# Performance work log

Hardware: AMD Instinct MI355X
Metric: run time of the kernel (lower is better)

The kernel has to match this reference:

```python
import jax, jax.numpy as jnp
import numpy as np

B, C, H, W = 4, 256, 64, 64
NB = 4            # num_bands
CR = C // 4       # channel-attention reduction


def _conv(x, w, b, pad):
    y = jax.lax.conv_general_dilated(x, w, window_strides=(1, 1),
                                     padding=[(pad, pad), (pad, pad)],
                                     dimension_numbers=('NCHW', 'OIHW', 'NCHW'))
    return y + b[None, :, None, None]


def setup_inputs() -> dict:
    key = jax.random.key(0)
    ks = jax.random.split(key, 16)
    d = {}
    d['x'] = jax.random.normal(ks[0], (B, C, H, W), dtype=jnp.float32)
    # spline weights / scalers: one (out,in) matrix per band
    d['spline_w'] = jax.random.normal(ks[1], (NB, C, C), dtype=jnp.float32) / np.sqrt(C)
    d['scalers'] = jax.random.uniform(ks[2], (NB, C, C), minval=0.9, maxval=1.1, dtype=jnp.float32)
    # feature_transform: conv3x3 -> BN -> ReLU -> conv3x3
    d['ft_w1'] = jax.random.normal(ks[3], (C, C, 3, 3), dtype=jnp.float32) / np.sqrt(C * 9)
    d['ft_b1'] = jnp.zeros((C,), jnp.float32)
    d['bn_g'] = jnp.ones((C,), jnp.float32)
    d['bn_b'] = jnp.zeros((C,), jnp.float32)
    d['bn_m'] = 0.01 * jax.random.normal(ks[4], (C,), dtype=jnp.float32)
    d['bn_v'] = jnp.ones((C,), jnp.float32)
    d['ft_w2'] = jax.random.normal(ks[5], (C, C, 3, 3), dtype=jnp.float32) / np.sqrt(C * 9)
    d['ft_b2'] = jnp.zeros((C,), jnp.float32)
    # channel attention: 1x1 convs C -> C/4 -> C
    d['ca_w1'] = jax.random.normal(ks[6], (CR, C, 1, 1), dtype=jnp.float32) / np.sqrt(C)
    d['ca_b1'] = jnp.zeros((CR,), jnp.float32)
    d['ca_w2'] = jax.random.normal(ks[7], (C, CR, 1, 1), dtype=jnp.float32) / np.sqrt(CR)
    d['ca_b2'] = jnp.zeros((C,), jnp.float32)
    # spatial attention: conv3x3 2 -> 1
    d['sa_w'] = jax.random.normal(ks[8], (1, 2, 3, 3), dtype=jnp.float32) / np.sqrt(18)
    d['sa_b'] = jnp.zeros((1,), jnp.float32)
    return d


def _forward(x, spline_w, scalers, ft_w1, ft_b1, bn_g, bn_b, bn_m, bn_v,
             ft_w2, ft_b2, ca_w1, ca_b1, ca_w2, ca_b2, sa_w, sa_b):
    eps = 1e-5

    def feature_transform(t):
        t = _conv(t, ft_w1, ft_b1, 1)
        t = bn_g[None, :, None, None] * (t - bn_m[None, :, None, None]) * \
            jax.lax.rsqrt(bn_v + eps)[None, :, None, None] + bn_b[None, :, None, None]
        t = jax.nn.relu(t)
        return _conv(t, ft_w2, ft_b2, 1)

    # ---- spectral decompose: rfft over channel dim, per-band irfft ----
    xf = x.transpose(0, 2, 3, 1).reshape(-1, C)      # (B*H*W, C)
    F = jnp.fft.rfft(xf, axis=-1)                    # (B*H*W, C//2+1)
    nfreq = F.shape[-1]
    bs = nfreq // NB
    bands = []
    for i in range(NB):
        s = i * bs
        e = nfreq if i == NB - 1 else (i + 1) * bs
        # irfft zero-pads the sliced spectrum back to length C (matches torch)
        bands.append(jnp.fft.irfft(F[:, s:e], n=C, axis=-1).reshape(B, H, W, C))
    xd = jnp.stack(bands, axis=1)                    # (B, NB, H, W, C)

    # NOTE: the original .view(B*NB, C, H, W) on a (B,NB,H,W,C)-contiguous tensor
    # is a raw memory reinterpretation (not a permute); jnp.reshape matches it.
    xd = xd.reshape(B * NB, C, H, W)
    xd = feature_transform(xd)
    xd = xd.reshape(B, NB, H, W, C)

    # ---- attention block (shares feature_transform weights) ----
    t = xd.reshape(B * NB, C, H, W)
    t = feature_transform(t)
    gap = jnp.mean(t, axis=(2, 3), keepdims=True)    # (B*NB, C, 1, 1)
    cw = jax.nn.sigmoid(_conv(jax.nn.gelu(_conv(gap, ca_w1, ca_b1, 0), approximate=False),
                              ca_w2, ca_b2, 0))
    t = t * cw
    avg_out = jnp.mean(t, axis=1, keepdims=True)
    max_out = jnp.max(t, axis=1, keepdims=True)
    sw = jax.nn.sigmoid(_conv(jnp.concatenate([avg_out, max_out], axis=1), sa_w, sa_b, 1))
    t = t * sw
    xd = t.reshape(B, NB, H, W, C)

    # ---- spline stage ----
    # In the source, the Cox-de Boor basis recursion is computed but UNUSED:
    # einsum('bci,oi->bci', band_x, weight) == band_x * weight.sum(0), so the
    # effective math is a per-band, per-feature scaling (dead basis code omitted).
    w_eff = (spline_w * scalers).sum(axis=1)          # (NB, C)
    xv = xd.reshape(B, NB, H * W, C)
    band_out = xv * w_eff[None, :, None, :]
    fused = band_out.mean(axis=1)                     # (B, H*W, C)
    return fused.reshape(B, H, W, C).transpose(0, 3, 1, 2)


def reference(x, spline_w, scalers, ft_w1, ft_b1, bn_g, bn_b, bn_m, bn_v,
              ft_w2, ft_b2, ca_w1, ca_b1, ca_w2, ca_b2, sa_w, sa_b):
    return _forward(x, spline_w, scalers, ft_w1, ft_b1, bn_g, bn_b, bn_m, bn_v,
                    ft_w2, ft_b2, ca_w1, ca_b1, ca_w2, ca_b2, sa_w, sa_b)
```

## Files before the change

kernel.cpp:

```cpp
#include <hip/hip_runtime.h>
#include <hip/hip_bf16.h>


#define CHW   1048576
#define HW    4096

typedef _Float16 f16;
typedef _Float16 f16x8 __attribute__((ext_vector_type(8)));
typedef float    f32x4 __attribute__((ext_vector_type(4)));

__global__ __launch_bounds__(256) void k2_kernel(float* __restrict__ K2) {
    __shared__ float ctab[256];
    const int c = blockIdx.x;
    const int t = threadIdx.x;
    ctab[t] = cosf((float)t * 0.024543692606170259f);
    __syncthreads();
#pragma unroll
    for (int q = 0; q < 4; q++) {
        const int o = q * 256 + t;
        const int s = q * 32;
        const int L = (q == 3) ? 33 : 32;
        float sum = ctab[(s * c) & 255];
        for (int k = 1; k < L; k++) {
            int m = ((s + k) * c + k * (256 - t)) & 255;
            sum += 2.f * ctab[m];
        }
        K2[c * 1024 + o] = sum * 0.00390625f;
    }
}

__global__ __launch_bounds__(256) void wsplit_kernel(const float* __restrict__ w,
                                                     f16* __restrict__ Wf) {
    const int tap = blockIdx.x / 16;
    const int ocgrp = blockIdx.x % 16;
    const int l = threadIdx.x & 63;
    const int c2 = threadIdx.x >> 6;
    const int lrow = l & 15, icg = l >> 4;
    const int oc = ocgrp * 16 + lrow;
#pragma unroll
    for (int s = 0; s < 2; ++s) {
        const int cc = c2 + s * 4;
        const int icb = cc * 32 + icg * 8;
        f16x8 hi, lo;
#pragma unroll
        for (int j = 0; j < 8; ++j) {
            float v = w[(oc * 256 + icb + j) * 9 + tap];
            f16 h = (f16)v;
            hi[j] = h;
            lo[j] = (f16)(v - (float)h);
        }
        const size_t base = (((size_t)(tap * 8 + cc) * 2) * 16 + ocgrp) * 512 +
                            (size_t)l * 8;
        *(f16x8*)&Wf[base] = hi;
        *(f16x8*)&Wf[base + 8192] = lo;
    }
}

__global__ __launch_bounds__(256) void small_pre_kernel(
    const float* __restrict__ spw, const float* __restrict__ scl,
    const float* __restrict__ bn_g, const float* __restrict__ bn_b,
    const float* __restrict__ bn_m, const float* __restrict__ bn_v,
    const float* __restrict__ ft_b1, float* __restrict__ weff,
    float* __restrict__ bnscale, float* __restrict__ bnbias) {
    const int c = threadIdx.x;
    const float s = bn_g[c] * rsqrtf(bn_v[c] + 1e-5f);
    bnscale[c] = s;
    bnbias[c] = (ft_b1[c] - bn_m[c]) * s + bn_b[c];
    for (int n = 0; n < 4; n++) {
        float acc = 0.f;
        for (int j = 0; j < 256; j++)
            acc += spw[n * 65536 + j * 256 + c] * scl[n * 65536 + j * 256 + c];
        weff[n * 256 + c] = acc;
    }
}

__global__ __launch_bounds__(256) void decompose_kernel(const float* __restrict__ x,
                                                        const float* __restrict__ K2,
                                                        float* __restrict__ xd) {
    const int o0 = blockIdx.x * 128;
    const int p0 = blockIdx.y * 64;
    const int b = p0 >> 12;
    const int prow = p0 & 4095;
    const int t = threadIdx.x;
    const int pg = t >> 4, og = t & 15;
    __shared__ float As[16][64];
    __shared__ float Bs[16][128];
    float acc[4][8];
#pragma unroll
    for (int i = 0; i < 4; i++)
#pragma unroll
        for (int j = 0; j < 8; j++) acc[i][j] = 0.f;

    for (int c0 = 0; c0 < 256; c0 += 16) {
#pragma unroll
        for (int i = 0; i < 4; i++) {
            int c = (t >> 6) + i * 4;
            As[c][t & 63] = x[b * CHW + (c0 + c) * HW + prow + (t & 63)];
        }
#pragma unroll
        for (int i = 0; i < 8; i++) {
            int l = i * 256 + t;
            Bs[l >> 7][l & 127] = K2[(c0 + (l >> 7)) * 1024 + o0 + (l & 127)];
        }
        __syncthreads();
#pragma unroll
        for (int k = 0; k < 16; k++) {
            float a[4], bb[8];
            *(float4*)a = *(const float4*)&As[k][pg * 4];
            *(float4*)&bb[0] = *(const float4*)&Bs[k][og * 8];
            *(float4*)&bb[4] = *(const float4*)&Bs[k][og * 8 + 4];
#pragma unroll
            for (int i = 0; i < 4; i++)
#pragma unroll
                for (int j = 0; j < 8; j++) acc[i][j] = fmaf(a[i], bb[j], acc[i][j]);
        }
        __syncthreads();
    }
#pragma unroll
    for (int i = 0; i < 4; i++) {
        const int p = prow + pg * 4 + i;
#pragma unroll
        for (int j = 0; j < 8; j++) {
            const int o = o0 + og * 8 + j;
            const int n = o >> 8, cc = o & 255;
            xd[b * 4194304 + n * CHW + p * 256 + cc] = acc[i][j];
        }
    }
}

__global__ __launch_bounds__(256) void xpose_kernel(const float* __restrict__ in,
                                                    f16* __restrict__ Xh,
                                                    f16* __restrict__ Xl) {
    const int bn = blockIdx.y;
    const int tid = blockIdx.x;
    const int k = tid & 15;
    const int cc0 = ((tid >> 4) & 1) * 128;
    const int c0p = (tid >> 5) * 64;
    __shared__ float T[64 * 132];
    const int base = bn * 1048576;
    for (int c = threadIdx.x; c < 2048; c += 256) {
        int cl = c >> 5;
        int ccq = c & 31;
        int pd = (c0p + cl) * 16 + k;
        *(float4*)&T[cl * 132 + ccq * 4] =
            *(const float4*)&in[base + pd * 256 + cc0 + ccq * 4];
    }
    __syncthreads();
    for (int m = threadIdx.x; m < 1024; m += 256) {
        int pl = m >> 3;
        int cq = m & 7;
        f16x8 hi, lo;
#pragma unroll
        for (int j = 0; j < 8; ++j) {
            float v = T[(cq * 8 + j) * 132 + pl];
            f16 h = (f16)v;
            hi[j] = h;
            lo[j] = (f16)(v - (float)h);
        }
        int pp = k * 256 + cc0 + pl;
        int o = base + pp * 256 + c0p + cq * 8;
        *(f16x8*)&Xh[o] = hi;
        *(f16x8*)&Xl[o] = lo;
    }
}

template <int MODE, int PACKED>
__global__ __launch_bounds__(256, 2) void conv_mfma_kernel(
    const f16* __restrict__ Xh, const f16* __restrict__ Xl,
    const f16* __restrict__ Wf,
    const float* __restrict__ scale, const float* __restrict__ bias,
    f16* __restrict__ Oh, f16* __restrict__ Ol, float* __restrict__ Of) {
    const int oc0 = blockIdx.x * 128;
    const int h0 = (blockIdx.y >> 2) * 8;
    const int w0 = (blockIdx.y & 3) * 16;
    const int bn = blockIdx.z;

    __shared__ __align__(16) f16 smem[16384];
    f16* At = smem;

    const int t = threadIdx.x;
    const int wid = t >> 6, lane = t & 63;
    const int wm = wid >> 1, wn = wid & 1;
    const int lrow = lane & 15, g = lane >> 4;

    const int row_s = t >> 3;
    const int sub_s = t & 7;
    const int half_s = sub_s >> 2, icq_s = sub_s & 3;
    const int swz_s = (sub_s ^ (row_s & 7)) << 3;

    f32x4 acc[4][4];
    const f32x4 z4 = {0.f, 0.f, 0.f, 0.f};
#pragma unroll
    for (int i = 0; i < 4; i++)
#pragma unroll
        for (int j = 0; j < 4; j++) acc[i][j] = z4;

    const int xbase = bn * CHW;

    const f16* wfb = Wf + ((size_t)((oc0 >> 4) + wn * 4)) * 512 + (size_t)lane * 8;

    f16x8 bh[2][4], bl[2][4];

#pragma unroll 1
    for (int chunk = 0; chunk < 8; ++chunk) {
        const int ic0 = chunk * 32;
        const int cbase = chunk * 16384;
        __syncthreads();
#pragma unroll
        for (int nf = 0; nf < 4; ++nf) {
            bh[0][nf] = *(const f16x8*)(wfb + cbase + nf * 512);
            bl[0][nf] = *(const f16x8*)(wfb + cbase + 8192 + nf * 512);
        }
        {
            const f16* xs = (half_s ? Xl : Xh) + xbase + ic0 + icq_s * 8;
#pragma unroll
            for (int i = 0; i < 7; ++i) {
                int c = t + i * 256;
                if (c < 1600) {
                    int pos = row_s + i * 32;
                    int r = pos / 20, col = pos - r * 20;
                    int gy = h0 - 1 + r, gx = w0 - 1 + col;
                    f16x8 v = {};
                    if (col < 18 && (unsigned)gy < 64u && (unsigned)gx < 64u)
                        v = *(const f16x8*)(xs + (gy * 64 + gx) * 256);
                    *(f16x8*)&At[pos * 64 + swz_s] = v;
                }
            }
        }
        __syncthreads();
#pragma unroll
        for (int tap = 0; tap < 9; ++tap) {
            const int ky = tap / 3, kx = tap % 3;
            const int pc = tap & 1;
            if (tap < 8) {
                const int off = (tap + 1) * 131072 + cbase;
#pragma unroll
                for (int nf = 0; nf < 4; ++nf) {
                    bh[pc ^ 1][nf] = *(const f16x8*)(wfb + off + nf * 512);
                    bl[pc ^ 1][nf] = *(const f16x8*)(wfb + off + 8192 + nf * 512);
                }
            }
            f16x8 a_h[4], a_l[4];
#pragma unroll
            for (int mf = 0; mf < 4; ++mf) {
                int pos = (wm * 4 + mf + ky) * 20 + (lrow + kx);
                int p7 = (pos & 7) << 3;
                a_h[mf] = *(const f16x8*)&At[pos * 64 + ((g << 3) ^ p7)];
                a_l[mf] = *(const f16x8*)&At[pos * 64 + (((4 + g) << 3) ^ p7)];
            }
#pragma unroll
            for (int mf = 0; mf < 4; ++mf)
#pragma unroll
                for (int nf = 0; nf < 4; ++nf) {
                    acc[mf][nf] = __builtin_amdgcn_mfma_f32_16x16x32_f16(
                        a_h[mf], bh[pc][nf], acc[mf][nf], 0, 0, 0);
                    acc[mf][nf] = __builtin_amdgcn_mfma_f32_16x16x32_f16(
                        a_h[mf], bl[pc][nf], acc[mf][nf], 0, 0, 0);
                    acc[mf][nf] = __builtin_amdgcn_mfma_f32_16x16x32_f16(
                        a_l[mf], bh[pc][nf], acc[mf][nf], 0, 0, 0);
                }
        }
    }

    if (PACKED == 0) {
#pragma unroll
        for (int nf = 0; nf < 4; ++nf) {
            const int oc = oc0 + wn * 64 + nf * 16 + lrow;
            const float sc = (MODE == 1) ? scale[oc] : 1.f;
            const float bi = bias[oc];
#pragma unroll
            for (int mf = 0; mf < 4; ++mf) {
                const int oh = wm * 4 + mf;
                float4 o;
                float* op = &o.x;
#pragma unroll
                for (int j = 0; j < 4; ++j) {
                    float v = acc[mf][nf][j];
                    op[j] = (MODE == 1) ? fmaxf(v * sc + bi, 0.f) : (v + bi);
                }
                *(float4*)&Of[bn * CHW + oc * HW + (h0 + oh) * 64 + w0 + g * 4] = o;
            }
        }
    } else {
        f16* Th = smem;
        f16* Tl = smem + 8192;
        for (int half = 0; half < 2; ++half) {
            __syncthreads();
            if (wn == half) {
#pragma unroll
                for (int nf = 0; nf < 4; ++nf) {
                    const int oclb = nf * 16 + lrow;
                    const int oc = oc0 + half * 64 + oclb;
                    const float sc = (MODE == 1) ? scale[oc] : 1.f;
                    const float bi = bias[oc];
#pragma unroll
                    for (int mf = 0; mf < 4; ++mf) {
                        const int pb = (wm * 4 + mf) * 16;
#pragma unroll
                        for (int j = 0; j < 4; ++j) {
                            float v = acc[mf][nf][j];
                            v = (MODE == 1) ? fmaxf(v * sc + bi, 0.f) : (v + bi);
                            f16 hi = (f16)v;
                            int p = pb + g * 4 + j;
                            int idx = p * 64 + (oclb ^ ((p & 7) << 3));
                            Th[idx] = hi;
                            Tl[idx] = (f16)(v - (float)hi);
                        }
                    }
                }
            }
            __syncthreads();
            for (int c = t; c < 1024; c += 256) {
                int p = c >> 3, q = c & 7;
                int src = p * 64 + ((q ^ (p & 7)) << 3);
                int gp = xbase + ((h0 + (p >> 4)) * 64 + w0 + (p & 15)) * 256 +
                         oc0 + half * 64 + q * 8;
                *(f16x8*)&Oh[gp] = *(const f16x8*)&Th[src];
                *(f16x8*)&Ol[gp] = *(const f16x8*)&Tl[src];
            }
        }
    }
}

__global__ __launch_bounds__(256) void gap_kernel(const float* __restrict__ t2,
                                                  float* __restrict__ gap) {
    const int bc = blockIdx.x;
    const float* p = t2 + bc * HW;
    float s = 0.f;
    for (int i = threadIdx.x; i < 4096; i += 256) s += p[i];
    __shared__ float red[256];
    red[threadIdx.x] = s;
    __syncthreads();
    for (int off = 128; off > 0; off >>= 1) {
        if (threadIdx.x < off) red[threadIdx.x] += red[threadIdx.x + off];
        __syncthreads();
    }
    if (threadIdx.x == 0) gap[bc] = red[0] * (1.f / 4096.f);
}

__global__ __launch_bounds__(256) void ca_kernel(
    const float* __restrict__ gap, const float* __restrict__ w1,
    const float* __restrict__ b1, const float* __restrict__ w2,
    const float* __restrict__ b2, float* __restrict__ cw) {
    const int bn = blockIdx.x;
    const int t = threadIdx.x;
    __shared__ float gsh[256];
    __shared__ float hid[64];
    gsh[t] = gap[bn * 256 + t];
    __syncthreads();
    if (t < 64) {
        float a = b1[t];
        for (int c = 0; c < 256; c++) a += w1[t * 256 + c] * gsh[c];
        hid[t] = 0.5f * a * (1.f + erff(a * 0.70710678118654752f));
    }
    __syncthreads();
    float a = b2[t];
    for (int j = 0; j < 64; j++) a += w2[t * 64 + j] * hid[j];
    cw[bn * 256 + t] = 1.f / (1.f + expf(-a));
}

__global__ __launch_bounds__(256) void samap_kernel(const float* __restrict__ t2,
                                                    const float* __restrict__ cw,
                                                    float* __restrict__ avg,
                                                    float* __restrict__ mx) {
    const int bn = blockIdx.x >> 4;
    const int h = (blockIdx.x & 15) * 4 + (threadIdx.x >> 6);
    const int w = threadIdx.x & 63;
    const float* p = t2 + bn * CHW + h * 64 + w;
    float s = 0.f, m = -3.4e38f;
    for (int c = 0; c < 256; c++) {
        float v = p[c * HW] * cw[bn * 256 + c];
        s += v;
        m = fmaxf(m, v);
    }
    avg[bn * HW + h * 64 + w] = s * (1.f / 256.f);
    mx[bn * HW + h * 64 + w] = m;
}

__global__ __launch_bounds__(256) void sw_kernel(const float* __restrict__ avg,
                                                 const float* __restrict__ mx,
                                                 const float* __restrict__ saw,
                                                 const float* __restrict__ sab,
                                                 float* __restrict__ sw) {
    const int bn = blockIdx.x >> 4;
    const int h = (blockIdx.x & 15) * 4 + (threadIdx.x >> 6);
    const int w = threadIdx.x & 63;
    float a = sab[0];
#pragma unroll
    for (int ky = 0; ky < 3; ky++) {
        int y = h + ky - 1;
        if ((unsigned)y >= 64u) continue;
#pragma unroll
        for (int kx = 0; kx < 3; kx++) {
            int x = w + kx - 1;
            if ((unsigned)x >= 64u) continue;
            int idx = bn * HW + y * 64 + x;
            a += saw[ky * 3 + kx] * avg[idx] + saw[9 + ky * 3 + kx] * mx[idx];
        }
    }
    sw[bn * HW + h * 64 + w] = 1.f / (1.f + expf(-a));
}

__global__ __launch_bounds__(256) void fuse_kernel(const float* __restrict__ t2,
                                                   const float* __restrict__ cw,
                                                   const float* __restrict__ sw,
                                                   const float* __restrict__ weff,
                                                   float* __restrict__ out) {
    const int b = blockIdx.x >> 6;
    const int ho = blockIdx.x & 63;
    const int co = threadIdx.x;
    __shared__ float T[256 * 33];
    float we[4];
#pragma unroll
    for (int n = 0; n < 4; n++) we[n] = weff[n * 256 + co];

    for (int hf = 0; hf < 2; hf++) {
        for (int wo = 0; wo < 32; wo++) {
            const int o = ho * 16384 + (hf * 32 + wo) * 256 + co;
            const int ct = o >> 12;
            const int ht = (o >> 6) & 63;
            const int wt = o & 63;
            float acc = 0.f;
#pragma unroll
            for (int n = 0; n < 4; n++) {
                const int bn = b * 4 + n;
                acc += we[n] * t2[bn * CHW + o] * cw[bn * 256 + ct] *
                       sw[bn * HW + ht * 64 + wt];
            }
            T[co * 33 + wo] = 0.25f * acc;
        }
        __syncthreads();
        for (int it = 0; it < 32; it++) {
            const int l = it * 256 + threadIdx.x;
            const int c2 = l >> 5, w2 = l & 31;
            out[b * CHW + c2 * HW + ho * 64 + hf * 32 + w2] = T[c2 * 33 + w2];
        }
        __syncthreads();
    }
}

extern "C" void kernel_launch(void* const* d_in, const int* in_sizes, int n_in,
                              void* d_out, int out_size, void* d_ws, size_t ws_size,
                              hipStream_t stream) {
    const float* x        = (const float*)d_in[0];
    const float* spline_w = (const float*)d_in[1];
    const float* scalers  = (const float*)d_in[2];
    const float* ft_w1    = (const float*)d_in[3];
    const float* ft_b1    = (const float*)d_in[4];
    const float* bn_g     = (const float*)d_in[5];
    const float* bn_b     = (const float*)d_in[6];
    const float* bn_m     = (const float*)d_in[7];
    const float* bn_v     = (const float*)d_in[8];
    const float* ft_w2    = (const float*)d_in[9];
    const float* ft_b2    = (const float*)d_in[10];
    const float* ca_w1    = (const float*)d_in[11];
    const float* ca_b1    = (const float*)d_in[12];
    const float* ca_w2    = (const float*)d_in[13];
    const float* ca_b2    = (const float*)d_in[14];
    const float* sa_w     = (const float*)d_in[15];
    const float* sa_b     = (const float*)d_in[16];

    char* p = (char*)d_ws;
    auto alloc = [&](size_t bytes) {
        char* r = p;
        p += (bytes + 255) & ~(size_t)255;
        return r;
    };
    float* K2      = (float*)alloc(262144 * 4);
    f16*   W1f     = (f16*)alloc((size_t)1179648 * 2);
    f16*   W2f     = (f16*)alloc((size_t)1179648 * 2);
    float* weff    = (float*)alloc(1024 * 4);
    float* bnscale = (float*)alloc(256 * 4);
    float* bnbias  = (float*)alloc(256 * 4);
    float* gapb    = (float*)alloc(4096 * 4);
    float* cwb     = (float*)alloc(4096 * 4);
    float* avgm    = (float*)alloc(65536 * 4);
    float* mxm     = (float*)alloc(65536 * 4);
    float* swm     = (float*)alloc(65536 * 4);
    const size_t HALF = (size_t)16777216 * 2;
    char* R1 = alloc(2 * HALF);
    char* R2 = alloc(2 * HALF);
    float* bufA = (float*)R1;
    f16*   Y1h  = (f16*)R1;
    f16*   Y1l  = (f16*)(R1 + HALF);
    f16*   X1h  = (f16*)R2;
    f16*   X1l  = (f16*)(R2 + HALF);
    f16*   Y2h  = (f16*)R2;
    f16*   Y2l  = (f16*)(R2 + HALF);
    float* t2   = (float*)R2;

    k2_kernel<<<256, 256, 0, stream>>>(K2);
    wsplit_kernel<<<144, 256, 0, stream>>>(ft_w1, W1f);
    wsplit_kernel<<<144, 256, 0, stream>>>(ft_w2, W2f);
    small_pre_kernel<<<1, 256, 0, stream>>>(spline_w, scalers, bn_g, bn_b, bn_m,
                                            bn_v, ft_b1, weff, bnscale, bnbias);
    decompose_kernel<<<dim3(8, 256), 256, 0, stream>>>(x, K2, bufA);
    xpose_kernel<<<dim3(128, 16), 256, 0, stream>>>(bufA, X1h, X1l);

    dim3 cgrid(2, 32, 16);
    conv_mfma_kernel<1, 1><<<cgrid, 256, 0, stream>>>(X1h, X1l, W1f,
                                                      bnscale, bnbias, Y1h, Y1l, nullptr);
    conv_mfma_kernel<0, 1><<<cgrid, 256, 0, stream>>>(Y1h, Y1l, W2f,
                                                      nullptr, ft_b2, Y2h, Y2l, nullptr);
    conv_mfma_kernel<1, 1><<<cgrid, 256, 0, stream>>>(Y2h, Y2l, W1f,
                                                      bnscale, bnbias, Y1h, Y1l, nullptr);
    conv_mfma_kernel<0, 0><<<cgrid, 256, 0, stream>>>(Y1h, Y1l, W2f,
                                                      nullptr, ft_b2, nullptr, nullptr, t2);

    gap_kernel<<<4096, 256, 0, stream>>>(t2, gapb);
    ca_kernel<<<16, 256, 0, stream>>>(gapb, ca_w1, ca_b1, ca_w2, ca_b2, cwb);
    samap_kernel<<<256, 256, 0, stream>>>(t2, cwb, avgm, mxm);
    sw_kernel<<<256, 256, 0, stream>>>(avgm, mxm, sa_w, sa_b, swm);
    fuse_kernel<<<256, 256, 0, stream>>>(t2, cwb, swm, weff, (float*)d_out);
}
```

Measured before the change: 1.071 ms.

## Double-buffer conv input tiles in LDS and prefetch next chunk into registers

The MFMA conv kernel now keeps two LDS buffers for the input halo tile. It loads the next channel chunk from global memory into registers while the current chunk's MFMAs run, then writes it into the other buffer afterwards, which drops one barrier per chunk. Weight-fragment prefetch now runs across chunk boundaries, and s_setprio raises wave priority around the MFMA block. The cost is a larger LDS footprint (about 50KB per block) and 7 extra f16x8 registers per thread, which may hurt occupancy at 2 blocks per CU.

New measurement: 1.296 ms. +21.1%, slower.

```diff
diff --git a/kernel.cpp b/kernel.cpp
--- a/kernel.cpp
+++ b/kernel.cpp
@@ -175,8 +175,7 @@
     const int w0 = (blockIdx.y & 3) * 16;
     const int bn = blockIdx.z;
 
-    __shared__ __align__(16) f16 smem[16384];
-    f16* At = smem;
+    __shared__ __align__(16) f16 smem[25600];
 
     const int t = threadIdx.x;
     const int wid = t >> 6, lane = t & 63;
@@ -200,40 +199,58 @@
     const f16* wfb = Wf + ((size_t)((oc0 >> 4) + wn * 4)) * 512 + (size_t)lane * 8;
 
     f16x8 bh[2][4], bl[2][4];
-
-#pragma unroll 1
+    f16x8 vA[7];
+
+#define LOADA(ch)                                                              \
+    {                                                                          \
+        const f16* xs = (half_s ? Xl : Xh) + xbase + (ch) * 32 + icq_s * 8;    \
+        _Pragma("unroll") for (int i = 0; i < 7; ++i) {                        \
+            int c = t + i * 256;                                               \
+            if (c < 1600) {                                                    \
+                int pos = row_s + i * 32;                                      \
+                int r = pos / 20, col = pos - r * 20;                          \
+                int gy = h0 - 1 + r, gx = w0 - 1 + col;                        \
+                f16x8 v = {};                                                  \
+                if (col < 18 && (unsigned)gy < 64u && (unsigned)gx < 64u)      \
+                    v = *(const f16x8*)(xs + (gy * 64 + gx) * 256);            \
+                vA[i] = v;                                                     \
+            }                                                                  \
+        }                                                                      \
+    }
+#define STOREA(buf)                                                            \
+    {                                                                          \
+        _Pragma("unroll") for (int i = 0; i < 7; ++i) {                        \
+            int c = t + i * 256;                                               \
+            if (c < 1600) {                                                    \
+                int pos = row_s + i * 32;                                      \
+                *(f16x8*)&(buf)[pos * 64 + swz_s] = vA[i];                     \
+            }                                                                  \
+        }                                                                      \
+    }
+
+#pragma unroll
+    for (int nf = 0; nf < 4; ++nf) {
+        bh[0][nf] = *(const f16x8*)(wfb + nf * 512);
+        bl[0][nf] = *(const f16x8*)(wfb + 8192 + nf * 512);
+    }
+    LOADA(0);
+    STOREA(smem);
+
+#pragma unroll 2
     for (int chunk = 0; chunk < 8; ++chunk) {
-        const int ic0 = chunk * 32;
+        f16* Acur = smem + (chunk & 1) * 12800;
+        f16* Anxt = smem + ((chunk & 1) ^ 1) * 12800;
         const int cbase = chunk * 16384;
         __syncthreads();
-#pragma unroll
-        for (int nf = 0; nf < 4; ++nf) {
-            bh[0][nf] = *(const f16x8*)(wfb + cbase + nf * 512);
-            bl[0][nf] = *(const f16x8*)(wfb + cbase + 8192 + nf * 512);
-        }
-        {
-            const f16* xs = (half_s ? Xl : Xh) + xbase + ic0 + icq_s * 8;
-#pragma unroll
-            for (int i = 0; i < 7; ++i) {
-                int c = t + i * 256;
-                if (c < 1600) {
-                    int pos = row_s + i * 32;
-                    int r = pos / 20, col = pos - r * 20;
-                    int gy = h0 - 1 + r, gx = w0 - 1 + col;
-                    f16x8 v = {};
-                    if (col < 18 && (unsigned)gy < 64u && (unsigned)gx < 64u)
-                        v = *(const f16x8*)(xs + (gy * 64 + gx) * 256);
-                    *(f16x8*)&At[pos * 64 + swz_s] = v;
-                }
-            }
-        }
-        __syncthreads();
+        if (chunk < 7) LOADA(chunk + 1);
 #pragma unroll
         for (int tap = 0; tap < 9; ++tap) {
             const int ky = tap / 3, kx = tap % 3;
-            const int pc = tap & 1;
-            if (tap < 8) {
-                const int off = (tap + 1) * 131072 + cbase;
+            const int pc = (chunk + tap) & 1;
+            int ntap = tap + 1, nch = chunk;
+            if (ntap == 9) { ntap = 0; nch = chunk + 1; }
+            if (nch < 8) {
+                const int off = ntap * 131072 + nch * 16384;
 #pragma unroll
                 for (int nf = 0; nf < 4; ++nf) {
                     bh[pc ^ 1][nf] = *(const f16x8*)(wfb + off + nf * 512);
@@ -245,9 +262,10 @@
             for (int mf = 0; mf < 4; ++mf) {
                 int pos = (wm * 4 + mf + ky) * 20 + (lrow + kx);
                 int p7 = (pos & 7) << 3;
-                a_h[mf] = *(const f16x8*)&At[pos * 64 + ((g << 3) ^ p7)];
-                a_l[mf] = *(const f16x8*)&At[pos * 64 + (((4 + g) << 3) ^ p7)];
+                a_h[mf] = *(const f16x8*)&Acur[pos * 64 + ((g << 3) ^ p7)];
+                a_l[mf] = *(const f16x8*)&Acur[pos * 64 + (((4 + g) << 3) ^ p7)];
             }
+            __builtin_amdgcn_s_setprio(1);
 #pragma unroll
             for (int mf = 0; mf < 4; ++mf)
 #pragma unroll
@@ -259,8 +277,12 @@
                     acc[mf][nf] = __builtin_amdgcn_mfma_f32_16x16x32_f16(
                         a_l[mf], bh[pc][nf], acc[mf][nf], 0, 0, 0);
                 }
-        }
-    }
+            __builtin_amdgcn_s_setprio(0);
+        }
+        if (chunk < 7) STOREA(Anxt);
+    }
+#undef LOADA
+#undef STOREA
 
     if (PACKED == 0) {
 #pragma unroll
```
